# Performance work log

Measured on AMD Instinct MI355X. Metric: run time of the kernel, lower is better.

The kernel has to match this reference:

```python
import jax, jax.numpy as jnp
import numpy as np

N = 500_000      # total observations
D = 40           # per-observation feature dim
S = 2048         # number of segments (time series)
WIDTH = 128      # psi hidden width
LATENT = 128     # latent width
DOT = 64         # dot_prod_dim
HEADS = 4        # n_heads


def setup_inputs() -> dict:
    key = jax.random.key(0)
    ks = jax.random.split(key, 12)

    def he(k, shape):
        fan_in = shape[0]
        lim = np.sqrt(6.0 / fan_in)
        return jax.random.uniform(k, shape, jnp.float32, -lim, lim)

    inputs = jax.random.normal(ks[0], (N, D), jnp.float32)
    segment_ids = jnp.sort(jax.random.randint(ks[1], (N,), 0, S))
    lengths = jax.random.randint(ks[2], (S,), 0, 300)
    return {
        "inputs": inputs,
        "segment_ids": segment_ids,
        "lengths": lengths,
        "W1": he(ks[3], (D, WIDTH)),      "b1": jnp.zeros((WIDTH,), jnp.float32),
        "W2": he(ks[4], (WIDTH, WIDTH)), "b2": jnp.zeros((WIDTH,), jnp.float32),
        "W3": he(ks[5], (WIDTH, LATENT)),"b3": jnp.zeros((LATENT,), jnp.float32),
        "Wr": he(ks[6], (LATENT, LATENT)),"br": jnp.zeros((LATENT,), jnp.float32),
        "W_k": he(ks[7], (LATENT + D, DOT * HEADS)),
        "W_q": jax.random.normal(ks[8], (HEADS, DOT), jnp.float32) * 0.02,
    }


def segment_softmax(x, seg, num_segments):
    # x: [N, H]; softmax over elements sharing the same segment id
    m = jax.ops.segment_max(x, seg, num_segments, indices_are_sorted=True)
    e = jnp.exp(x - m[seg])
    denom = jax.ops.segment_sum(e, seg, num_segments, indices_are_sorted=True)
    return e / denom[seg]


def reference(inputs, segment_ids, lengths, W1, b1, W2, b2, W3, b3, Wr, br, W_k, W_q):
    relu = jax.nn.relu
    # psi: 2 hidden dense layers + latent projection (all relu)
    h = relu(inputs @ W1 + b1)
    h = relu(h @ W2 + b2)
    enc = relu(h @ W3 + b3)                                   # [N, LATENT]
    # segment mean aggregation
    sums = jax.ops.segment_sum(enc, segment_ids, S, indices_are_sorted=True)
    counts = jax.ops.segment_sum(jnp.ones((enc.shape[0], 1), enc.dtype),
                                 segment_ids, S, indices_are_sorted=True)
    agg = sums / jnp.maximum(counts, 1.0)                      # [S, LATENT]
    agg = relu(agg @ Wr + br)                                  # rho
    # broadcast back and combine
    combined = jnp.concatenate([inputs, agg[segment_ids]], axis=-1)  # [N, D+LATENT]
    keys = (combined @ W_k).reshape(-1, HEADS, DOT)            # split+stack == reshape
    preattn = jnp.einsum('nhd,hd->nh', keys, W_q) / jnp.sqrt(jnp.float32(DOT))
    attn = segment_softmax(preattn, segment_ids, S)            # [N, H]
    # match original: list of per-head [N, 1] tensors -> stacked [H, N, 1]
    return jnp.transpose(attn)[..., None]
```

## Files before the change

kernel.cpp:

```cpp
#include <hip/hip_runtime.h>
#include <math.h>


#define NROWS 500000
#define DIM 40
#define NSEG 2048
#define DOTD 64
#define NH 4
#define BLOCK 256
#define SEG_PER_BLOCK 4
#define CACHE_IT 24
#define NEG_INF (-3.0e38f)

__global__ __launch_bounds__(BLOCK) void prep_kernel(
    const int* __restrict__ seg,
    const float* __restrict__ Wk,
    const float* __restrict__ Wq,
    int* __restrict__ seg_start,
    int* __restrict__ seg_end,
    float* __restrict__ wxg)
{
    const int tid = (int)threadIdx.x;
    const int n = (int)(blockIdx.x * BLOCK + tid);

    if (blockIdx.x == 0 && tid < DIM * NH) {
        const int d = tid >> 2;
        const int h = tid & 3;
        const float* wkp = Wk + d * (NH * DOTD) + h * DOTD;
        const float* wqp = Wq + h * DOTD;
        float acc = 0.f;
        #pragma unroll
        for (int j = 0; j < DOTD; ++j) acc += wkp[j] * wqp[j];
        wxg[tid] = acc * 0.125f;
    }

    if (n < NROWS) {
        const int s = seg[n];
        if (n == 0) {
            seg_start[s] = 0;
            for (int t = 0; t < s; ++t) { seg_start[t] = 0; seg_end[t] = 0; }
        } else {
            const int sp = seg[n - 1];
            if (sp != s) {
                seg_start[s] = n;
                seg_end[sp] = n;
                for (int t = sp + 1; t < s; ++t) { seg_start[t] = n; seg_end[t] = n; }
            }
        }
        if (n == NROWS - 1) {
            seg_end[s] = NROWS;
            for (int t = s + 1; t < NSEG; ++t) { seg_start[t] = NROWS; seg_end[t] = NROWS; }
        }
    }
}

__device__ __forceinline__ float quad_logit(
    const float* __restrict__ x, const float (*wx)[NH],
    int n, int jj, bool valid)
{
    float acc[NH] = {0.f, 0.f, 0.f, 0.f};
    if (valid) {
        const float2* p = (const float2*)(x + (size_t)n * DIM);
        #pragma unroll
        for (int k = 0; k < 5; ++k) {
            const float2 v = p[jj + 4 * k];
            const int d0 = 2 * (jj + 4 * k);
            #pragma unroll
            for (int h = 0; h < NH; ++h) {
                acc[h] += v.x * wx[d0][h] + v.y * wx[d0 + 1][h];
            }
        }
    }
    #pragma unroll
    for (int h = 0; h < NH; ++h) {
        acc[h] += __shfl_xor(acc[h], 1, 64);
        acc[h] += __shfl_xor(acc[h], 2, 64);
    }
    const float t0 = (jj & 1) ? acc[1] : acc[0];
    const float t1 = (jj & 1) ? acc[3] : acc[2];
    return (jj & 2) ? t1 : t0;
}

__global__ __launch_bounds__(BLOCK) void seg_attn_kernel(
    const float* __restrict__ x,
    const int* __restrict__ seg_start,
    const int* __restrict__ seg_end,
    const float* __restrict__ wxg,
    float* __restrict__ out)
{
    __shared__ float wx[DIM][NH];

    const int tid = (int)threadIdx.x;
    if (tid < DIM * NH) wx[tid >> 2][tid & 3] = wxg[tid];
    __syncthreads();

    const int lane = tid & 63;
    const int g = lane >> 2;
    const int jj = lane & 3;
    const int s = (int)blockIdx.x * SEG_PER_BLOCK + (tid >> 6);
    const int start = seg_start[s];
    const int end = seg_end[s];
    const int rows = end - start;
    if (rows <= 0) return;
    const int iters = (rows + 15) >> 4;

    float cache[CACHE_IT];
    float lmax = NEG_INF;
    for (int it = 0; it < iters; ++it) {
        const int r = it * 16 + g;
        const bool valid = (r < rows);
        float l = quad_logit(x, wx, start + r, jj, valid);
        if (!valid) l = NEG_INF;
        if (it < CACHE_IT) cache[it] = l;
        lmax = fmaxf(lmax, l);
    }

    float m = lmax;
    #pragma unroll
    for (int off = 4; off <= 32; off <<= 1) m = fmaxf(m, __shfl_xor(m, off, 64));

    float lsum = 0.f;
    for (int it = 0; it < iters; ++it) {
        float e;
        if (it < CACHE_IT) {
            e = __expf(cache[it] - m);
            cache[it] = e;
        } else {
            const int r = it * 16 + g;
            const bool valid = (r < rows);
            float l = quad_logit(x, wx, start + r, jj, valid);
            e = valid ? __expf(l - m) : 0.f;
        }
        lsum += e;
    }
    float v = lsum;
    #pragma unroll
    for (int off = 4; off <= 32; off <<= 1) v += __shfl_xor(v, off, 64);
    const float rden = 1.0f / v;

    for (int it = 0; it < iters; ++it) {
        const int r = it * 16 + g;
        if (r >= rows) continue;
        float e;
        if (it < CACHE_IT) {
            e = cache[it];
        } else {
            float l = quad_logit(x, wx, start + r, jj, true);
            e = __expf(l - m);
        }
        out[(size_t)jj * NROWS + start + r] = e * rden;
    }
}

extern "C" void kernel_launch(void* const* d_in, const int* in_sizes, int n_in,
                              void* d_out, int out_size, void* d_ws, size_t ws_size,
                              hipStream_t stream) {
    const float* x  = (const float*)d_in[0];
    const int* seg  = (const int*)d_in[1];
    const float* Wk = (const float*)d_in[11];
    const float* Wq = (const float*)d_in[12];
    float* out = (float*)d_out;

    int* seg_start = (int*)d_ws;
    int* seg_end   = seg_start + NSEG;
    float* wxg     = (float*)(seg_end + NSEG);

    hipLaunchKernelGGL(prep_kernel, dim3((NROWS + BLOCK - 1) / BLOCK), dim3(BLOCK),
                       0, stream, seg, Wk, Wq, seg_start, seg_end, wxg);
    hipLaunchKernelGGL(seg_attn_kernel, dim3(NSEG / SEG_PER_BLOCK), dim3(BLOCK),
                       0, stream, x, seg_start, seg_end, wxg, out);
}
```

Before: 148.1 us.

## Replace per-segment softmax with flat row-parallel exp plus atomic segment sums

Replaces the one-wavefront-per-segment softmax with a row-parallel logits kernel. Each thread computes its row's four head logits using float4 loads, exponentiates them without subtracting the segment max, and stores them to a workspace buffer. Per-segment denominators come from a wave-level segmented scan followed by atomicAdds, and a final elementwise kernel normalizes. This removes the load imbalance and low occupancy of per-segment waves and drops the max pass. It adds an extra read and write of the exp buffer, and it risks overflow or precision loss if logits are large, since the max-stabilization is gone.

```diff
diff --git a/kernel.cpp b/kernel.cpp
--- a/kernel.cpp
+++ b/kernel.cpp
@@ -8,148 +8,100 @@
 #define DOTD 64
 #define NH 4
 #define BLOCK 256
-#define SEG_PER_BLOCK 4
-#define CACHE_IT 24
-#define NEG_INF (-3.0e38f)
 
-__global__ __launch_bounds__(BLOCK) void prep_kernel(
-    const int* __restrict__ seg,
+__global__ __launch_bounds__(BLOCK) void prep0_kernel(
     const float* __restrict__ Wk,
     const float* __restrict__ Wq,
-    int* __restrict__ seg_start,
-    int* __restrict__ seg_end,
+    float* __restrict__ denom,
     float* __restrict__ wxg)
 {
-    const int tid = (int)threadIdx.x;
-    const int n = (int)(blockIdx.x * BLOCK + tid);
-
-    if (blockIdx.x == 0 && tid < DIM * NH) {
-        const int d = tid >> 2;
-        const int h = tid & 3;
+    const int t = (int)(blockIdx.x * BLOCK + threadIdx.x);
+    if (t < NSEG * NH) denom[t] = 0.f;
+    if (blockIdx.x == 32 && threadIdx.x < DIM * NH) {
+        const int d = (int)threadIdx.x >> 2;
+        const int h = (int)threadIdx.x & 3;
         const float* wkp = Wk + d * (NH * DOTD) + h * DOTD;
         const float* wqp = Wq + h * DOTD;
         float acc = 0.f;
         #pragma unroll
         for (int j = 0; j < DOTD; ++j) acc += wkp[j] * wqp[j];
-        wxg[tid] = acc * 0.125f;
-    }
-
-    if (n < NROWS) {
-        const int s = seg[n];
-        if (n == 0) {
-            seg_start[s] = 0;
-            for (int t = 0; t < s; ++t) { seg_start[t] = 0; seg_end[t] = 0; }
-        } else {
-            const int sp = seg[n - 1];
-            if (sp != s) {
-                seg_start[s] = n;
-                seg_end[sp] = n;
-                for (int t = sp + 1; t < s; ++t) { seg_start[t] = n; seg_end[t] = n; }
-            }
-        }
-        if (n == NROWS - 1) {
-            seg_end[s] = NROWS;
-            for (int t = s + 1; t < NSEG; ++t) { seg_start[t] = NROWS; seg_end[t] = NROWS; }
-        }
+        wxg[threadIdx.x] = acc * 0.125f;
     }
 }
 
-__device__ __forceinline__ float quad_logit(
-    const float* __restrict__ x, const float (*wx)[NH],
-    int n, int jj, bool valid)
+__global__ __launch_bounds__(BLOCK) void logits_kernel(
+    const float* __restrict__ x,
+    const int* __restrict__ seg,
+    const float* __restrict__ wxg,
+    float4* __restrict__ e4,
+    float* __restrict__ denom)
 {
-    float acc[NH] = {0.f, 0.f, 0.f, 0.f};
+    __shared__ float wx[DIM][NH];
+    const int tid = (int)threadIdx.x;
+    if (tid < DIM * NH) ((float*)wx)[tid] = wxg[tid];
+    __syncthreads();
+
+    const int n = (int)(blockIdx.x * BLOCK + tid);
+    const bool valid = (n < NROWS);
+    const int s = valid ? seg[n] : -1;
+
+    float e[NH] = {0.f, 0.f, 0.f, 0.f};
     if (valid) {
-        const float2* p = (const float2*)(x + (size_t)n * DIM);
+        const float4* xr = (const float4*)(x + (size_t)n * DIM);
+        float acc[NH] = {0.f, 0.f, 0.f, 0.f};
         #pragma unroll
-        for (int k = 0; k < 5; ++k) {
-            const float2 v = p[jj + 4 * k];
-            const int d0 = 2 * (jj + 4 * k);
+        for (int q = 0; q < DIM / 4; ++q) {
+            const float4 v = xr[q];
             #pragma unroll
             for (int h = 0; h < NH; ++h) {
-                acc[h] += v.x * wx[d0][h] + v.y * wx[d0 + 1][h];
+                acc[h] += v.x * wx[4 * q + 0][h];
+                acc[h] += v.y * wx[4 * q + 1][h];
+                acc[h] += v.z * wx[4 * q + 2][h];
+                acc[h] += v.w * wx[4 * q + 3][h];
             }
         }
+        #pragma unroll
+        for (int h = 0; h < NH; ++h) e[h] = __expf(acc[h]);
+        float4 ev;
+        ev.x = e[0]; ev.y = e[1]; ev.z = e[2]; ev.w = e[3];
+        e4[n] = ev;
     }
+
+    const int lane = tid & 63;
+    const int snext = __shfl_down(s, 1, 64);
+    const bool tail = (lane == 63) || (snext != s);
+
+    float v[NH] = {e[0], e[1], e[2], e[3]};
     #pragma unroll
-    for (int h = 0; h < NH; ++h) {
-        acc[h] += __shfl_xor(acc[h], 1, 64);
-        acc[h] += __shfl_xor(acc[h], 2, 64);
+    for (int off = 1; off <= 32; off <<= 1) {
+        const int su = __shfl_up(s, off, 64);
+        #pragma unroll
+        for (int h = 0; h < NH; ++h) {
+            const float u = __shfl_up(v[h], off, 64);
+            if (lane >= off && su == s) v[h] += u;
+        }
     }
-    const float t0 = (jj & 1) ? acc[1] : acc[0];
-    const float t1 = (jj & 1) ? acc[3] : acc[2];
-    return (jj & 2) ? t1 : t0;
+    if (tail && valid) {
+        #pragma unroll
+        for (int h = 0; h < NH; ++h) atomicAdd(&denom[s * NH + h], v[h]);
+    }
 }
 
-__global__ __launch_bounds__(BLOCK) void seg_attn_kernel(
-    const float* __restrict__ x,
-    const int* __restrict__ seg_start,
-    const int* __restrict__ seg_end,
-    const float* __restrict__ wxg,
+__global__ __launch_bounds__(BLOCK) void norm_kernel(
+    const int* __restrict__ seg,
+    const float4* __restrict__ e4,
+    const float* __restrict__ denom,
     float* __restrict__ out)
 {
-    __shared__ float wx[DIM][NH];
-
-    const int tid = (int)threadIdx.x;
-    if (tid < DIM * NH) wx[tid >> 2][tid & 3] = wxg[tid];
-    __syncthreads();
-
-    const int lane = tid & 63;
-    const int g = lane >> 2;
-    const int jj = lane & 3;
-    const int s = (int)blockIdx.x * SEG_PER_BLOCK + (tid >> 6);
-    const int start = seg_start[s];
-    const int end = seg_end[s];
-    const int rows = end - start;
-    if (rows <= 0) return;
-    const int iters = (rows + 15) >> 4;
-
-    float cache[CACHE_IT];
-    float lmax = NEG_INF;
-    for (int it = 0; it < iters; ++it) {
-        const int r = it * 16 + g;
-        const bool valid = (r < rows);
-        float l = quad_logit(x, wx, start + r, jj, valid);
-        if (!valid) l = NEG_INF;
-        if (it < CACHE_IT) cache[it] = l;
-        lmax = fmaxf(lmax, l);
-    }
-
-    float m = lmax;
-    #pragma unroll
-    for (int off = 4; off <= 32; off <<= 1) m = fmaxf(m, __shfl_xor(m, off, 64));
-
-    float lsum = 0.f;
-    for (int it = 0; it < iters; ++it) {
-        float e;
-        if (it < CACHE_IT) {
-            e = __expf(cache[it] - m);
-            cache[it] = e;
-        } else {
-            const int r = it * 16 + g;
-            const bool valid = (r < rows);
-            float l = quad_logit(x, wx, start + r, jj, valid);
-            e = valid ? __expf(l - m) : 0.f;
-        }
-        lsum += e;
-    }
-    float v = lsum;
-    #pragma unroll
-    for (int off = 4; off <= 32; off <<= 1) v += __shfl_xor(v, off, 64);
-    const float rden = 1.0f / v;
-
-    for (int it = 0; it < iters; ++it) {
-        const int r = it * 16 + g;
-        if (r >= rows) continue;
-        float e;
-        if (it < CACHE_IT) {
-            e = cache[it];
-        } else {
-            float l = quad_logit(x, wx, start + r, jj, true);
-            e = __expf(l - m);
-        }
-        out[(size_t)jj * NROWS + start + r] = e * rden;
-    }
+    const int n = (int)(blockIdx.x * BLOCK + threadIdx.x);
+    if (n >= NROWS) return;
+    const int s = seg[n];
+    const float4 e = e4[n];
+    const float4 d = *(const float4*)(denom + s * NH);
+    out[(size_t)0 * NROWS + n] = e.x / d.x;
+    out[(size_t)1 * NROWS + n] = e.y / d.y;
+    out[(size_t)2 * NROWS + n] = e.z / d.z;
+    out[(size_t)3 * NROWS + n] = e.w / d.w;
 }
 
 extern "C" void kernel_launch(void* const* d_in, const int* in_sizes, int n_in,
@@ -161,12 +113,15 @@
     const float* Wq = (const float*)d_in[12];
     float* out = (float*)d_out;
 
-    int* seg_start = (int*)d_ws;
-    int* seg_end   = seg_start + NSEG;
-    float* wxg     = (float*)(seg_end + NSEG);
+    float* denom = (float*)d_ws;
+    float* wxg   = denom + NSEG * NH;
+    float4* e4   = (float4*)((char*)d_ws + 65536);
 
-    hipLaunchKernelGGL(prep_kernel, dim3((NROWS + BLOCK - 1) / BLOCK), dim3(BLOCK),
-                       0, stream, seg, Wk, Wq, seg_start, seg_end, wxg);
-    hipLaunchKernelGGL(seg_attn_kernel, dim3(NSEG / SEG_PER_BLOCK), dim3(BLOCK),
-                       0, stream, x, seg_start, seg_end, wxg, out);
+    const int rowblocks = (NROWS + BLOCK - 1) / BLOCK;
+    hipLaunchKernelGGL(prep0_kernel, dim3(33), dim3(BLOCK), 0, stream,
+                       Wk, Wq, denom, wxg);
+    hipLaunchKernelGGL(logits_kernel, dim3(rowblocks), dim3(BLOCK), 0, stream,
+                       x, seg, wxg, e4, denom);
+    hipLaunchKernelGGL(norm_kernel, dim3(rowblocks), dim3(BLOCK), 0, stream,
+                       seg, e4, denom, out);
 }
```

New measurement: 148.9 us. Within noise of the previous version (+0.6%).
